# Performance work log

Hardware: AMD Instinct MI355X
Metric: run time of the kernel (lower is better)

Reference implementation:

```python
import jax, jax.numpy as jnp
import numpy as np

B, S, D = 4, 2048, 1024
H, HD = 16, 64  # num_heads, head_size
NEG = -1e20


def setup_inputs() -> dict:
    key = jax.random.key(0)
    ks = jax.random.split(key, 8)
    query = jax.random.normal(ks[0], (B, S, D), dtype=jnp.float32)
    k_in = jax.random.normal(ks[1], (B, S, D), dtype=jnp.float32)
    v_in = jax.random.normal(ks[2], (B, S, D), dtype=jnp.float32)
    # causal mask: True where attention is DISALLOWED (masked_fill semantics)
    mask = jnp.triu(jnp.ones((S, S), dtype=bool), k=1)
    scale = 1.0 / np.sqrt(D)
    Wq = jax.random.normal(ks[3], (D, H * HD), dtype=jnp.float32) * scale
    Wk = jax.random.normal(ks[4], (D, H * HD), dtype=jnp.float32) * scale
    Wv = jax.random.normal(ks[5], (D, H * HD), dtype=jnp.float32) * scale
    Wo = jax.random.normal(ks[6], (H * HD, D), dtype=jnp.float32) * scale
    bo = jnp.zeros((D,), dtype=jnp.float32)
    return {"query": query, "key": k_in, "value": v_in, "mask": mask,
            "Wq": Wq, "Wk": Wk, "Wv": Wv, "Wo": Wo, "bo": bo}


def reference(query, key, value, mask, Wq, Wk, Wv, Wo, bo):
    # projections -> [B, H, S, HD]
    q = (query @ Wq).reshape(B, -1, H, HD).transpose(0, 2, 1, 3)
    k = (key @ Wk).reshape(B, -1, H, HD).transpose(0, 2, 1, 3)
    v = (value @ Wv).reshape(B, -1, H, HD).transpose(0, 2, 1, 3)
    # scaled dot-product attention with boolean mask (True = masked out)
    scores = jnp.einsum('bhqd,bhkd->bhqk', q, k) / jnp.sqrt(jnp.float32(HD))
    scores = jnp.where(mask, jnp.float32(NEG), scores)
    attn = jax.nn.softmax(scores, axis=-1)
    out = jnp.einsum('bhqk,bhkd->bhqd', attn, v)  # [B,H,S,HD]
    out = out.transpose(0, 2, 1, 3).reshape(B, -1, H * HD)
    return out @ Wo + bo
```

## Files before the change

### kernel.cpp

```cpp
#include <hip/hip_runtime.h>

#define B_ 4
#define S_ 2048
#define D_ 1024
#define H_ 16
#define HD_ 64

typedef __attribute__((ext_vector_type(8))) short bf16x8;
typedef __attribute__((ext_vector_type(4))) float f32x4;

__device__ __forceinline__ short f2bf(float f) {
  unsigned u = __builtin_bit_cast(unsigned, f);
  u += 0x7fffu + ((u >> 16) & 1u);
  return (short)(u >> 16);
}

__device__ __forceinline__ unsigned cvtpk(float a, float b) {
  unsigned r;
  asm("v_cvt_pk_bf16_f32 %0, %1, %2" : "=v"(r) : "v"(a), "v"(b));
  return r;
}

__device__ __forceinline__ void gload_lds16(const void* g, void* l) {
  __builtin_amdgcn_global_load_lds((const __attribute__((address_space(1))) void*)g,
                                   (__attribute__((address_space(3))) void*)l, 16, 0, 0);
}

__device__ __forceinline__ bf16x8 ldsw8(const short* base, int row, int colb) {
  const int off = (row * 128 + colb) ^ ((row & 7) << 4);
  return *(const bf16x8*)((const char*)base + off);
}

#define MFMA16(a, b, c) __builtin_amdgcn_mfma_f32_16x16x32_bf16((a), (b), (c), 0, 0, 0)
#define PBAR()   asm volatile("s_barrier" ::: "memory")
#define LGKM0()  do { asm volatile("s_waitcnt lgkmcnt(0)" ::: "memory"); \
                      __builtin_amdgcn_sched_barrier(0); } while (0)

__global__ void transpose_cast_w4(const float* __restrict__ W0, const float* __restrict__ W1,
                                  const float* __restrict__ W2, const float* __restrict__ W3,
                                  short* __restrict__ T0, short* __restrict__ T1,
                                  short* __restrict__ T2, short* __restrict__ T3) {
  __shared__ float tile[32][33];
  const int z = blockIdx.z;
  const float* W = z == 0 ? W0 : z == 1 ? W1 : z == 2 ? W2 : W3;
  short* Wt = z == 0 ? T0 : z == 1 ? T1 : z == 2 ? T2 : T3;
  const int n0 = blockIdx.x * 32, k0 = blockIdx.y * 32;
  const int tx = threadIdx.x, ty = threadIdx.y;
  #pragma unroll
  for (int i = ty; i < 32; i += 8)
    tile[i][tx] = W[(size_t)(k0 + i) * 1024 + n0 + tx];
  __syncthreads();
  #pragma unroll
  for (int i = ty; i < 32; i += 8)
    Wt[(size_t)(n0 + i) * 1024 + k0 + tx] = f2bf(tile[tx][i]);
}

__global__ void cast3(const float* __restrict__ q, const float* __restrict__ k,
                      const float* __restrict__ v, short* __restrict__ oq,
                      short* __restrict__ ok, short* __restrict__ ov) {
  const int z = blockIdx.z;
  const float* in = z == 0 ? q : z == 1 ? k : v;
  short* out = z == 0 ? oq : z == 1 ? ok : ov;
  const int i = blockIdx.x * 256 + threadIdx.x;
  const float4 f = ((const float4*)in)[i];
  ((uint2*)out)[i] = make_uint2(cvtpk(f.x, f.y), cvtpk(f.z, f.w));
}

template <int MODE>
__global__ __launch_bounds__(512, 2) void gemm8(const short* __restrict__ A0p,
                                                const short* __restrict__ A1p,
                                                const short* __restrict__ A2p,
                                                const short* __restrict__ Bt0,
                                                const short* __restrict__ Bt1,
                                                const short* __restrict__ Bt2,
                                                short* __restrict__ O0,
                                                short* __restrict__ O1,
                                                short* __restrict__ O2,
                                                float* __restrict__ outf,
                                                const float* __restrict__ bias,
                                                float qscale) {
  __shared__ __align__(16) short lds[2][4][8192];
  const int z = (MODE == 0) ? blockIdx.z : 0;
  const short* A = z == 0 ? A0p : z == 1 ? A1p : A2p;
  const short* Bt = z == 0 ? Bt0 : z == 1 ? Bt1 : Bt2;
  short* outb = z == 0 ? O0 : z == 1 ? O1 : O2;
  const float oscale = (MODE == 0 && z == 0) ? qscale : 1.0f;

  const int tid = threadIdx.x;
  const int l = tid & 63, w = tid >> 6;
  const int wm = w >> 2, wn = w & 3;
  const int l15 = l & 15, lq = l >> 4;
  const int flat = blockIdx.x + (blockIdx.y << 2);
  const int vid = (flat & 7) * 16 + (flat >> 3);
  const int row0 = (vid >> 2) * 256;
  const int col0 = (vid & 3) * 256;

  f32x4 acc[8][4] = {};

  auto stageH = [&](short* dst, const short* src, int rbase, int hrow, int kt) {
    #pragma unroll
    for (int j = 0; j < 2; ++j) {
      const int o2 = w * 1024 + j * 8192 + l * 16;
      const int row = o2 >> 7;
      const int sc = (o2 & 127) ^ ((row & 7) << 4);
      gload_lds16((const char*)src + ((size_t)(rbase + hrow + row) * 1024 + kt * 64) * 2 + sc,
                  (char*)dst + o2);
    }
  };

  stageH(lds[0][2], Bt, col0, 0, 0);
  stageH(lds[0][3], Bt, col0, 128, 0);
  stageH(lds[0][0], A, row0, 0, 0);
  stageH(lds[0][1], A, row0, 128, 0);
  stageH(lds[1][2], Bt, col0, 0, 1);
  stageH(lds[1][3], Bt, col0, 128, 1);

  for (int t = 0; t < 16; ++t) {
    const int c = t & 1, o = c ^ 1;
    if (t < 15) asm volatile("s_waitcnt vmcnt(4)" ::: "memory");
    else        asm volatile("s_waitcnt vmcnt(0)" ::: "memory");
    PBAR();

    const short* Ah = lds[c][wm];
    const short* Bh = lds[c][2 + (wn >> 1)];
    const int brow = (wn & 1) * 64;
    bf16x8 bfr[4][2];

    #pragma unroll
    for (int p = 0; p < 4; ++p) {
      if (p == 0 && t + 1 < 16) stageH(lds[o][0], A, row0, 0, t + 1);
      if (p == 1 && t + 1 < 16) stageH(lds[o][1], A, row0, 128, t + 1);
      if (p == 1 && t + 2 < 16) stageH(lds[c][2], Bt, col0, 0, t + 2);
      if (p == 2 && t + 2 < 16) stageH(lds[c][3], Bt, col0, 128, t + 2);

      if (p == 0) {
        #pragma unroll
        for (int nf = 0; nf < 4; ++nf)
          #pragma unroll
          for (int ks = 0; ks < 2; ++ks)
            bfr[nf][ks] = ldsw8(Bh, brow + nf * 16 + l15, ks * 64 + lq * 16);
      }
      const bf16x8 a00 = ldsw8(Ah, (2 * p) * 16 + l15, lq * 16);
      const bf16x8 a01 = ldsw8(Ah, (2 * p) * 16 + l15, 64 + lq * 16);
      const bf16x8 a10 = ldsw8(Ah, (2 * p + 1) * 16 + l15, lq * 16);
      const bf16x8 a11 = ldsw8(Ah, (2 * p + 1) * 16 + l15, 64 + lq * 16);

      LGKM0();
      __builtin_amdgcn_s_setprio(1);
      #pragma unroll
      for (int nf = 0; nf < 4; ++nf) {
        acc[2 * p][nf]     = MFMA16(a00, bfr[nf][0], acc[2 * p][nf]);
        acc[2 * p][nf]     = MFMA16(a01, bfr[nf][1], acc[2 * p][nf]);
        acc[2 * p + 1][nf] = MFMA16(a10, bfr[nf][0], acc[2 * p + 1][nf]);
        acc[2 * p + 1][nf] = MFMA16(a11, bfr[nf][1], acc[2 * p + 1][nf]);
      }
      __builtin_amdgcn_s_setprio(0);
      PBAR();
    }
  }

  #pragma unroll
  for (int mf = 0; mf < 8; ++mf) {
    #pragma unroll
    for (int nf = 0; nf < 4; ++nf) {
      #pragma unroll
      for (int r = 0; r < 4; ++r) {
        const int gr = row0 + wm * 128 + mf * 16 + lq * 4 + r;
        const int gc = col0 + wn * 64 + nf * 16 + l15;
        const float v = acc[mf][nf][r];
        if (MODE == 0) {
          const int b = gr >> 11, s = gr & 2047;
          const int h = gc >> 6, hd = gc & 63;
          if (z < 2)
            outb[(((size_t)(b * H_ + h)) * S_ + s) * HD_ + hd] = f2bf(v * oscale);
          else
            outb[(((size_t)(b * H_ + h)) * HD_ + hd) * S_ + s] = f2bf(v);
        } else {
          outf[(size_t)gr * 1024 + gc] = v + bias[gc];
        }
      }
    }
  }
}

__global__ __launch_bounds__(256) void attn_kernel(const short* __restrict__ Qh,
                                                   const short* __restrict__ Kh,
                                                   const short* __restrict__ Vtr,
                                                   short* __restrict__ attnout) {
  __shared__ __align__(16) short Ks[2][64 * 64];
  __shared__ __align__(16) short Vs[2][64 * 64];
  __shared__ __align__(16) short Ps[4][32 * 64];
  const int tid = threadIdx.x, l = tid & 63, w = tid >> 6;
  const int l15 = l & 15, lq = l >> 4;
  const int flat = blockIdx.x;
  const int vid = (flat & 7) * 64 + (flat >> 3);
  const int bh = vid >> 3, pairx = vid & 7;
  const int b = bh >> 4, h = bh & 15;
  const size_t base = (size_t)bh * (S_ * HD_);
  const short* Qp = Qh + base;
  const short* Kp = Kh + base;
  const short* Vp = Vtr + base;
  short* Pw = (short*)Ps[w];

  for (int pass = 0; pass < 2; ++pass) {
    const int qt = pass ? 15 - pairx : pairx;
    const int q0 = qt * 128;
    const int qw = q0 + w * 32;
    const int nkt = (q0 >> 6) + 2;

    bf16x8 qf[2][2];
    #pragma unroll
    for (int qh = 0; qh < 2; qh++)
      #pragma unroll
      for (int ks = 0; ks < 2; ks++)
        qf[qh][ks] = *(const bf16x8*)(Qp + (size_t)(qw + qh * 16 + l15) * 64 + ks * 32 + lq * 8);

    f32x4 oacc[4][2] = {};
    float mrow[2] = {-1e30f, -1e30f};
    float lpart[2] = {0.f, 0.f};

    auto stage = [&](int kt, int bf) {
      const int k0s = kt << 6;
      #pragma unroll
      for (int i = 0; i < 2; i++) {
        const int o = w * 2048 + i * 1024 + l * 16;
        const int sw = o ^ (((o >> 7) & 7) << 4);
        gload_lds16((const char*)Kp + (size_t)k0s * 128 + sw, (char*)Ks[bf] + o);
        gload_lds16(Vp + (size_t)(o >> 7) * S_ + k0s + ((sw & 127) >> 1), (char*)Vs[bf] + o);
      }
    };

    stage(0, 0);
    __syncthreads();

    for (int kt = 0; kt < nkt; ++kt) {
      const int cur = kt & 1;
      if (kt + 1 < nkt) stage(kt + 1, cur ^ 1);
      const int k0 = kt << 6;

      if (k0 <= qw + 31) {
        f32x4 sacc[2][4] = {};
        __builtin_amdgcn_s_setprio(1);
        #pragma unroll
        for (int ks = 0; ks < 2; ks++) {
          #pragma unroll
          for (int mf = 0; mf < 4; mf++) {
            const bf16x8 kf = ldsw8(Ks[cur], mf * 16 + l15, ks * 64 + lq * 16);
            #pragma unroll
            for (int qh = 0; qh < 2; qh++)
              sacc[qh][mf] = MFMA16(kf, qf[qh][ks], sacc[qh][mf]);
          }
        }
        __builtin_amdgcn_s_setprio(0);

        if (k0 + 63 > qw) {
          #pragma unroll
          for (int qh = 0; qh < 2; qh++) {
            const int qg = qw + qh * 16 + l15 - lq * 4;
            #pragma unroll
            for (int mf = 0; mf < 4; mf++)
              #pragma unroll
              for (int r = 0; r < 4; r++)
                if (k0 + mf * 16 + r > qg) sacc[qh][mf][r] = -1e30f;
          }
        }

        float mxl[2];
        #pragma unroll
        for (int qh = 0; qh < 2; qh++) {
          float m = fmaxf(fmaxf(sacc[qh][0][0], sacc[qh][0][1]),
                          fmaxf(sacc[qh][0][2], sacc[qh][0][3]));
          #pragma unroll
          for (int mf = 1; mf < 4; mf++)
            m = fmaxf(m, fmaxf(fmaxf(sacc[qh][mf][0], sacc[qh][mf][1]),
                               fmaxf(sacc[qh][mf][2], sacc[qh][mf][3])));
          mxl[qh] = m;
        }

        const bool need = (mxl[0] > mrow[0] + 8.f) || (mxl[1] > mrow[1] + 8.f);
        if (__any(need)) {
          #pragma unroll
          for (int qh = 0; qh < 2; qh++) {
            float m = fmaxf(mxl[qh], __shfl_xor(mxl[qh], 16));
            m = fmaxf(m, __shfl_xor(m, 32));
            const float mn = fmaxf(mrow[qh], m);
            const float fac = __builtin_amdgcn_exp2f(mrow[qh] - mn);
            mrow[qh] = mn;
            lpart[qh] *= fac;
            #pragma unroll
            for (int mf = 0; mf < 4; mf++) oacc[mf][qh] *= fac;
          }
        }

        #pragma unroll
        for (int qh = 0; qh < 2; qh++) {
          float rs = 0.f;
          const int row = qh * 16 + l15;
          #pragma unroll
          for (int mf = 0; mf < 4; mf++) {
            f32x4 p;
            #pragma unroll
            for (int r = 0; r < 4; r++) {
              const float e = __builtin_amdgcn_exp2f(sacc[qh][mf][r] - mrow[qh]);
              p[r] = e;
              rs += e;
            }
            const int off = (row * 128 + mf * 32 + lq * 8) ^ ((row & 7) << 4);
            *(uint2*)((char*)Pw + off) = make_uint2(cvtpk(p[0], p[1]), cvtpk(p[2], p[3]));
          }
          lpart[qh] += rs;
        }

        asm volatile("s_waitcnt lgkmcnt(0)" ::: "memory");
        __builtin_amdgcn_sched_barrier(0);

        __builtin_amdgcn_s_setprio(1);
        #pragma unroll
        for (int ks = 0; ks < 2; ks++) {
          bf16x8 pb[2];
          #pragma unroll
          for (int qh = 0; qh < 2; qh++) {
            const int row = qh * 16 + l15;
            const int off = (row * 128 + ks * 64 + lq * 16) ^ ((row & 7) << 4);
            pb[qh] = *(const bf16x8*)((const char*)Pw + off);
          }
          #pragma unroll
          for (int mf = 0; mf < 4; mf++) {
            const bf16x8 vf = ldsw8(Vs[cur], mf * 16 + l15, ks * 64 + lq * 16);
            #pragma unroll
            for (int qh = 0; qh < 2; qh++)
              oacc[mf][qh] = MFMA16(vf, pb[qh], oacc[mf][qh]);
          }
        }
        __builtin_amdgcn_s_setprio(0);
      }
      __syncthreads();
    }

    #pragma unroll
    for (int qh = 0; qh < 2; qh++) {
      float lr = lpart[qh];
      lr += __shfl_xor(lr, 16);
      lr += __shfl_xor(lr, 32);
      const float rinv = __builtin_amdgcn_rcpf(lr);
      const int q = qw + qh * 16 + l15;
      #pragma unroll
      for (int mf = 0; mf < 4; mf++) {
        const f32x4 o = oacc[mf][qh];
        const uint2 u = make_uint2(cvtpk(o[0] * rinv, o[1] * rinv),
                                   cvtpk(o[2] * rinv, o[3] * rinv));
        *(uint2*)(attnout + ((size_t)b * S_ + q) * (H_ * HD_) + h * 64 + mf * 16 + lq * 4) = u;
      }
    }
  }
}

extern "C" void kernel_launch(void* const* d_in, const int* in_sizes, int n_in,
                              void* d_out, int out_size, void* d_ws, size_t ws_size,
                              hipStream_t stream) {
  const float* query = (const float*)d_in[0];
  const float* key_  = (const float*)d_in[1];
  const float* value = (const float*)d_in[2];
  const float* Wq = (const float*)d_in[4];
  const float* Wk = (const float*)d_in[5];
  const float* Wv = (const float*)d_in[6];
  const float* Wo = (const float*)d_in[7];
  const float* bo = (const float*)d_in[8];
  float* out = (float*)d_out;

  char* ws = (char*)d_ws;
  const size_t MB = (size_t)1 << 20;
  short* Aq   = (short*)(ws);
  short* Ak   = (short*)(ws + 16 * MB);
  short* Av   = (short*)(ws + 32 * MB);
  short* Xbuf = (short*)(ws);
  short* Wqt  = (short*)(ws + 48 * MB);
  short* Wkt  = (short*)(ws + 50 * MB);
  short* Wvt  = (short*)(ws + 52 * MB);
  short* Wot  = (short*)(ws + 54 * MB);
  short* Qh   = (short*)(ws + 56 * MB);
  short* Kh   = (short*)(ws + 72 * MB);
  short* Vt   = (short*)(ws + 88 * MB);

  const dim3 tb(32, 8);
  const dim3 tg4(32, 32, 4);
  const float QSCALE = 0.125f * 1.4426950408889634f;

  transpose_cast_w4<<<tg4, tb, 0, stream>>>(Wq, Wk, Wv, Wo, Wqt, Wkt, Wvt, Wot);

  cast3<<<dim3(8192, 1, 3), 256, 0, stream>>>(query, key_, value, Aq, Ak, Av);

  gemm8<0><<<dim3(4, 32, 3), 512, 0, stream>>>(Aq, Ak, Av, Wqt, Wkt, Wvt,
                                               Qh, Kh, Vt, nullptr, nullptr, QSCALE);

  attn_kernel<<<dim3(512), 256, 0, stream>>>(Qh, Kh, Vt, Xbuf);

  gemm8<1><<<dim3(4, 32, 1), 512, 0, stream>>>(Xbuf, nullptr, nullptr, Wot, nullptr, nullptr,
                                               nullptr, nullptr, nullptr, out, bo, 1.0f);
}
```

Measured before the change: 220.5 us.

## Replace output-projection GEMM with smaller-tile 128x128 kernel for more blocks

The output projection no longer reuses the 256x256-tile gemm8 template, which launched only 128 blocks for an 8192x1024 GEMM. It now uses a dedicated gemm_o kernel with 128x128 tiles, 256 threads, K-step 32 and double-buffered LDS loaded via global_load_lds with a paired-row swizzle, giving 512 blocks. The aim is better CU occupancy on the final GEMM. The cost is less data reuse per tile and a short per-iteration K loop with a __syncthreads each step.

```diff
diff --git a/kernel.cpp b/kernel.cpp
--- a/kernel.cpp
+++ b/kernel.cpp
@@ -29,6 +29,10 @@
 __device__ __forceinline__ bf16x8 ldsw8(const short* base, int row, int colb) {
   const int off = (row * 128 + colb) ^ ((row & 7) << 4);
   return *(const bf16x8*)((const char*)base + off);
+}
+
+__device__ __forceinline__ int bpr_off(int row, int cbyte) {
+  return ((row >> 1) << 7) + ((((row & 1) << 6) + cbyte) ^ (((row >> 1) & 7) << 4));
 }
 
 #define MFMA16(a, b, c) __builtin_amdgcn_mfma_f32_16x16x32_bf16((a), (b), (c), 0, 0, 0)
@@ -66,7 +70,6 @@
   ((uint2*)out)[i] = make_uint2(cvtpk(f.x, f.y), cvtpk(f.z, f.w));
 }
 
-template <int MODE>
 __global__ __launch_bounds__(512, 2) void gemm8(const short* __restrict__ A0p,
                                                 const short* __restrict__ A1p,
                                                 const short* __restrict__ A2p,
@@ -76,15 +79,13 @@
                                                 short* __restrict__ O0,
                                                 short* __restrict__ O1,
                                                 short* __restrict__ O2,
-                                                float* __restrict__ outf,
-                                                const float* __restrict__ bias,
                                                 float qscale) {
   __shared__ __align__(16) short lds[2][4][8192];
-  const int z = (MODE == 0) ? blockIdx.z : 0;
+  const int z = blockIdx.z;
   const short* A = z == 0 ? A0p : z == 1 ? A1p : A2p;
   const short* Bt = z == 0 ? Bt0 : z == 1 ? Bt1 : Bt2;
   short* outb = z == 0 ? O0 : z == 1 ? O1 : O2;
-  const float oscale = (MODE == 0 && z == 0) ? qscale : 1.0f;
+  const float oscale = (z == 0) ? qscale : 1.0f;
 
   const int tid = threadIdx.x;
   const int l = tid & 63, w = tid >> 6;
@@ -168,19 +169,83 @@
         const int gr = row0 + wm * 128 + mf * 16 + lq * 4 + r;
         const int gc = col0 + wn * 64 + nf * 16 + l15;
         const float v = acc[mf][nf][r];
-        if (MODE == 0) {
-          const int b = gr >> 11, s = gr & 2047;
-          const int h = gc >> 6, hd = gc & 63;
-          if (z < 2)
-            outb[(((size_t)(b * H_ + h)) * S_ + s) * HD_ + hd] = f2bf(v * oscale);
-          else
-            outb[(((size_t)(b * H_ + h)) * HD_ + hd) * S_ + s] = f2bf(v);
-        } else {
-          outf[(size_t)gr * 1024 + gc] = v + bias[gc];
-        }
+        const int b = gr >> 11, s = gr & 2047;
+        const int h = gc >> 6, hd = gc & 63;
+        if (z < 2)
+          outb[(((size_t)(b * H_ + h)) * S_ + s) * HD_ + hd] = f2bf(v * oscale);
+        else
+          outb[(((size_t)(b * H_ + h)) * HD_ + hd) * S_ + s] = f2bf(v);
       }
     }
   }
+}
+
+__global__ __launch_bounds__(256) void gemm_o(const short* __restrict__ A,
+                                              const short* __restrict__ Bt,
+                                              float* __restrict__ outf,
+                                              const float* __restrict__ bias) {
+  __shared__ __align__(16) short As[2][128 * 32];
+  __shared__ __align__(16) short Bs[2][128 * 32];
+  const int tid = threadIdx.x;
+  const int l = tid & 63;
+  const int w = tid >> 6;
+  const int wm = w >> 1, wn = w & 1;
+  const int flat = blockIdx.x + (blockIdx.y << 3);
+  const int xcd = flat & 7, t = flat >> 3;
+  const int row0 = (xcd * 8 + (t & 7)) * 128;
+  const int col0 = (t >> 3) * 128;
+  const int l15 = l & 15, lq = l >> 4;
+
+  f32x4 acc[4][4] = {};
+
+  auto stage = [&](const short* src, int r0, int k0, short* lds) {
+    #pragma unroll
+    for (int i = 0; i < 2; i++) {
+      const int o = w * 2048 + i * 1024 + l * 16;
+      const int row2 = o >> 7;
+      const int ip = (o & 127) ^ ((row2 & 7) << 4);
+      const int row = row2 * 2 + (ip >> 6);
+      const int cb = ip & 63;
+      gload_lds16((const char*)src + ((size_t)(r0 + row) * 1024 + k0) * 2 + cb,
+                  (char*)lds + o);
+    }
+  };
+
+  stage(A, row0, 0, As[0]);
+  stage(Bt, col0, 0, Bs[0]);
+
+  for (int kt = 0; kt < 32; ++kt) {
+    __syncthreads();
+    if (kt + 1 < 32) {
+      stage(A, row0, (kt + 1) * 32, As[(kt + 1) & 1]);
+      stage(Bt, col0, (kt + 1) * 32, Bs[(kt + 1) & 1]);
+    }
+    const short* as = As[kt & 1];
+    const short* bs = Bs[kt & 1];
+    bf16x8 af[4], bfv[4];
+    #pragma unroll
+    for (int mf = 0; mf < 4; mf++)
+      af[mf] = *(const bf16x8*)((const char*)as + bpr_off(wm * 64 + mf * 16 + l15, lq * 16));
+    #pragma unroll
+    for (int nf = 0; nf < 4; nf++)
+      bfv[nf] = *(const bf16x8*)((const char*)bs + bpr_off(wn * 64 + nf * 16 + l15, lq * 16));
+    #pragma unroll
+    for (int mf = 0; mf < 4; mf++)
+      #pragma unroll
+      for (int nf = 0; nf < 4; nf++)
+        acc[mf][nf] = MFMA16(af[mf], bfv[nf], acc[mf][nf]);
+  }
+
+  #pragma unroll
+  for (int mf = 0; mf < 4; mf++)
+    #pragma unroll
+    for (int nf = 0; nf < 4; nf++)
+      #pragma unroll
+      for (int r = 0; r < 4; r++) {
+        const int gr = row0 + wm * 64 + mf * 16 + lq * 4 + r;
+        const int gc = col0 + wn * 64 + nf * 16 + l15;
+        outf[(size_t)gr * 1024 + gc] = acc[mf][nf][r] + bias[gc];
+      }
 }
 
 __global__ __launch_bounds__(256) void attn_kernel(const short* __restrict__ Qh,
@@ -390,11 +455,10 @@
 
   cast3<<<dim3(8192, 1, 3), 256, 0, stream>>>(query, key_, value, Aq, Ak, Av);
 
-  gemm8<0><<<dim3(4, 32, 3), 512, 0, stream>>>(Aq, Ak, Av, Wqt, Wkt, Wvt,
-                                               Qh, Kh, Vt, nullptr, nullptr, QSCALE);
+  gemm8<<<dim3(4, 32, 3), 512, 0, stream>>>(Aq, Ak, Av, Wqt, Wkt, Wvt,
+                                            Qh, Kh, Vt, QSCALE);
 
   attn_kernel<<<dim3(512), 256, 0, stream>>>(Qh, Kh, Vt, Xbuf);
 
-  gemm8<1><<<dim3(4, 32, 1), 512, 0, stream>>>(Xbuf, nullptr, nullptr, Wot, nullptr, nullptr,
-                                               nullptr, nullptr, nullptr, out, bo, 1.0f);
-}
+  gemm_o<<<dim3(8, 64), 256, 0, stream>>>(Xbuf, Wot, out, bo);
+}
```

Measured after the change: 218.9 us. About the same (-0.7%).
